# Kernel tuning notes

Measured on AMD Instinct MI355X. Metric: run time of the kernel, lower is better.

## Reference

```python
import jax, jax.numpy as jnp
import numpy as np

B_, L_, D_MODEL = 2, 4096, 1024
D_STATE, D_CONV, D_INNER = 64, 4, 2048
EPS = 1.1920929e-07  # torch.finfo(float32).eps, nn.RMSNorm default


def setup_inputs() -> dict:
    key = jax.random.key(0)
    ks = jax.random.split(key, 8)
    s = 0.02
    x = jax.random.normal(ks[0], (B_, L_, D_MODEL), jnp.float32)
    W_in = jax.random.normal(ks[1], (D_MODEL, 2 * D_INNER), jnp.float32) * s
    conv_w = jax.random.normal(ks[2], (D_INNER, 1, D_CONV), jnp.float32) * s  # depthwise (O,I/g,K)
    conv_b = jnp.zeros((D_INNER,), jnp.float32)
    W_x = jax.random.normal(ks[3], (D_INNER, 2 * D_STATE + D_INNER), jnp.float32) * s
    W_dt = jax.random.normal(ks[4], (D_INNER, D_INNER), jnp.float32) * s
    b_dt = jnp.zeros((D_INNER,), jnp.float32)
    A_log = jnp.log(jnp.tile(jnp.arange(1, D_STATE + 1, dtype=jnp.float32)[None, :], (D_INNER, 1)))
    D_param = jnp.ones((D_INNER,), jnp.float32)
    W_out = jax.random.normal(ks[5], (D_INNER, D_MODEL), jnp.float32) * s
    norm_w = jnp.ones((D_INNER,), jnp.float32)
    return dict(x=x, W_in=W_in, conv_w=conv_w, conv_b=conv_b, W_x=W_x, W_dt=W_dt,
                b_dt=b_dt, A_log=A_log, D_param=D_param, W_out=W_out, norm_w=norm_w)


def selective_scan(x_conv, dt, A, B_ssm, C_ssm, D_param):
    # x_conv,dt: (B,L,d_inner); A:(d_inner,d_state); B_ssm,C_ssm:(B,L,d_state)
    dt = jax.nn.softplus(dt)

    def step(h, inp):
        dt_t, B_t, C_t, x_t = inp  # (B,di),(B,ds),(B,ds),(B,di)
        dA = jnp.exp(dt_t[:, :, None] * A[None, :, :])           # (B,di,ds)
        h = dA * h + (dt_t * x_t)[:, :, None] * B_t[:, None, :]  # (B,di,ds)
        y = jnp.einsum('bds,bs->bd', h, C_t)                     # (B,di)
        return h, y

    h0 = jnp.zeros((x_conv.shape[0], A.shape[0], A.shape[1]), x_conv.dtype)
    xs = (jnp.moveaxis(dt, 1, 0), jnp.moveaxis(B_ssm, 1, 0),
          jnp.moveaxis(C_ssm, 1, 0), jnp.moveaxis(x_conv, 1, 0))
    _, ys = jax.lax.scan(step, h0, xs)
    y = jnp.moveaxis(ys, 0, 1)  # (B,L,d_inner)
    return y + x_conv * D_param[None, None, :]


def reference(x, W_in, conv_w, conv_b, W_x, W_dt, b_dt, A_log, D_param, W_out, norm_w):
    xz = x @ W_in                                    # (B,L,2*d_inner)
    x_ssm, z = jnp.split(xz, 2, axis=-1)
    # causal depthwise conv1d: left-pad d_conv-1 == torch pad-both-then-slice[:L]
    xc = jnp.swapaxes(x_ssm, 1, 2)                   # (B,d_inner,L)
    xc = jax.lax.conv_general_dilated(
        xc, conv_w, window_strides=(1,), padding=[(D_CONV - 1, 0)],
        dimension_numbers=('NCH', 'OIH', 'NCH'), feature_group_count=D_INNER)
    xc = xc + conv_b[None, :, None]
    xc = jax.nn.silu(jnp.swapaxes(xc, 1, 2))         # (B,L,d_inner)
    dbc = xc @ W_x                                   # (B,L,2*d_state+d_inner)
    B_ssm = dbc[..., :D_STATE]
    C_ssm = dbc[..., D_STATE:2 * D_STATE]
    dt = dbc[..., 2 * D_STATE:] @ W_dt + b_dt
    A = -jnp.exp(A_log)
    y = selective_scan(xc, dt, A, B_ssm, C_ssm, D_param)
    # RMSNorm then gate
    y = y * jax.lax.rsqrt(jnp.mean(y * y, axis=-1, keepdims=True) + EPS) * norm_w
    y = y * jax.nn.silu(z)
    return y @ W_out
```

## Files before the change

### kernel.cpp

```cpp
#include <hip/hip_runtime.h>
#include <hip/hip_bf16.h>

#define L_SEQ   4096
#define DMODEL  1024
#define DINNER  2048
#define DSTATE  64
#define NB      2
#define DPB     128
#define DBCS    2304
#define NROWS   (NB * L_SEQ)

typedef unsigned short u16;
typedef __attribute__((ext_vector_type(8))) short bf16x8;
typedef __attribute__((ext_vector_type(4))) float f32x4;
typedef __attribute__((ext_vector_type(2))) float f32x2;

__device__ __forceinline__ float silu_f(float x)  { return x / (1.f + __expf(-x)); }
__device__ __forceinline__ float softplus_f(float x) {
    return x > 15.f ? x : __logf(1.f + __expf(x));
}
__device__ __forceinline__ float bf2f(u16 u) { return __uint_as_float(((unsigned)u) << 16); }
__device__ __forceinline__ u16 f2bf(float f) {
    __hip_bfloat16 h = __float2bfloat16(f);
    return *reinterpret_cast<u16*>(&h);
}
__device__ __forceinline__ unsigned pack2(float a, float b) {
    return (unsigned)f2bf(a) | ((unsigned)f2bf(b) << 16);
}

__global__ __launch_bounds__(256) void f32_to_bf16_kernel(
    const float* __restrict__ in, u16* __restrict__ out)
{
    const int i = (blockIdx.x * 256 + threadIdx.x) * 4;
    float4 v = *reinterpret_cast<const float4*>(in + i);
    ushort4 o;
    o.x = f2bf(v.x); o.y = f2bf(v.y); o.z = f2bf(v.z); o.w = f2bf(v.w);
    *reinterpret_cast<ushort4*>(out + i) = o;
}

__global__ __launch_bounds__(256) void transpose_bf16_kernel(
    const float* __restrict__ W, u16* __restrict__ Wt, int K, int N)
{
    __shared__ float t[32][33];
    const int n0 = blockIdx.x * 32, k0 = blockIdx.y * 32;
    const int tx = threadIdx.x & 31, ty = threadIdx.x >> 5;
    #pragma unroll
    for (int i = 0; i < 32; i += 8)
        t[ty + i][tx] = W[(size_t)(k0 + ty + i) * N + n0 + tx];
    __syncthreads();
    #pragma unroll
    for (int i = 0; i < 32; i += 8)
        Wt[(size_t)(n0 + ty + i) * K + k0 + tx] = f2bf(t[tx][ty + i]);
}

__global__ __launch_bounds__(256) void bias_cat_kernel(
    const float* __restrict__ b_dt, float* __restrict__ bias)
{
    const int i = blockIdx.x * 256 + threadIdx.x;
    float v = 0.f;
    if (i >= 128 && i < 128 + DINNER) v = b_dt[i - 128];
    bias[i] = v;
}

#define BAR()  asm volatile("s_barrier" ::: "memory")
#define WV(n)  asm volatile("s_waitcnt vmcnt(" #n ")" ::: "memory")
#define STG16(s, d) __builtin_amdgcn_global_load_lds( \
    (const __attribute__((address_space(1))) void*)(s), \
    (__attribute__((address_space(3))) void*)(d), 16, 0, 0)

template <typename TC, int ACT>
__global__ __launch_bounds__(512, 2) void gemm256(
    const u16* __restrict__ A, int lda,
    const u16* __restrict__ Bt, int ldb,
    TC* __restrict__ C, int ldc,
    int K, const float* __restrict__ bias)
{
    extern __shared__ char lds[];
    const int tid = threadIdx.x;
    const int l = tid & 63, w = tid >> 6;
    const int wm = w >> 2, wn = w & 3;
    const int lr = l & 15, lk = l >> 4;

    const int gx = gridDim.x;
    const int nwg = gx * gridDim.y;
    int wg = blockIdx.y * gx + blockIdx.x;
    wg = (wg & 7) * (nwg >> 3) + (wg >> 3);
    const int bm = (wg / gx) * 256, bn = (wg % gx) * 256;

    const size_t ldaB = (size_t)lda * 2, ldbB = (size_t)ldb * 2;
    const int gsw = (((l & 7) ^ (l >> 3)) << 4);
    const char* aSrc = (const char*)A + (size_t)(bm + w * 8 + (l >> 3)) * ldaB + gsw;
    const char* bSrc = (const char*)Bt + (size_t)(bn + w * 8 + (l >> 3)) * ldbB + gsw;
    const int csw0 = (lk * 16) ^ ((lr & 7) << 4);
    const int wdst = w * 1024;

    const int nk = K >> 6;
    f32x4 acc[8][4] = {};

    {
        STG16(aSrc + (size_t)(0 * 64) * ldaB, lds + 0 * 8192 + wdst);
        STG16(aSrc + (size_t)(2 * 64) * ldaB, lds + 2 * 8192 + wdst);
        STG16(bSrc + (size_t)(0 * 64) * ldbB, lds + 32768 + 0 * 8192 + wdst);
        STG16(bSrc + (size_t)(1 * 64) * ldbB, lds + 32768 + 1 * 8192 + wdst);
        STG16(bSrc + (size_t)(2 * 64) * ldbB, lds + 32768 + 2 * 8192 + wdst);
        STG16(bSrc + (size_t)(3 * 64) * ldbB, lds + 32768 + 3 * 8192 + wdst);
        STG16(aSrc + (size_t)(1 * 64) * ldaB, lds + 1 * 8192 + wdst);
        STG16(aSrc + (size_t)(3 * 64) * ldaB, lds + 3 * 8192 + wdst);
        WV(2);
        BAR();
    }

    for (int t = 0; t < nk; ++t) {
        const int p = t & 1;
        const char* Ar = lds + (p << 16);
        const char* Br = Ar + 32768;
        const int tn = (t + 1 < nk) ? t + 1 : t;
        char* dq = lds + (((t + 1) & 1) << 16);
        const size_t Tb = (size_t)tn << 7;
        const char* aS = aSrc + Tb;
        const char* bS = bSrc + Tb;

        bf16x8 a[4][2], bf[2][2];

        #pragma unroll
        for (int mi = 0; mi < 4; ++mi) {
            const int ro = (wm * 128 + mi * 16 + lr) * 128;
            a[mi][0] = *reinterpret_cast<const bf16x8*>(Ar + ro + csw0);
            a[mi][1] = *reinterpret_cast<const bf16x8*>(Ar + ro + (csw0 ^ 64));
        }
        #pragma unroll
        for (int ni = 0; ni < 2; ++ni) {
            const int ro = (wn * 64 + ni * 16 + lr) * 128;
            bf[ni][0] = *reinterpret_cast<const bf16x8*>(Br + ro + csw0);
            bf[ni][1] = *reinterpret_cast<const bf16x8*>(Br + ro + (csw0 ^ 64));
        }
        STG16(aS + (size_t)(0 * 64) * ldaB, dq + 0 * 8192 + wdst);
        STG16(aS + (size_t)(2 * 64) * ldaB, dq + 2 * 8192 + wdst);
        BAR();
        __builtin_amdgcn_s_setprio(1);
        #pragma unroll
        for (int mi = 0; mi < 4; ++mi)
            #pragma unroll
            for (int ni = 0; ni < 2; ++ni) {
                acc[mi][ni] = __builtin_amdgcn_mfma_f32_16x16x32_bf16(a[mi][0], bf[ni][0], acc[mi][ni], 0, 0, 0);
                acc[mi][ni] = __builtin_amdgcn_mfma_f32_16x16x32_bf16(a[mi][1], bf[ni][1], acc[mi][ni], 0, 0, 0);
            }
        __builtin_amdgcn_s_setprio(0);
        BAR();

        #pragma unroll
        for (int ni = 0; ni < 2; ++ni) {
            const int ro = (wn * 64 + (2 + ni) * 16 + lr) * 128;
            bf[ni][0] = *reinterpret_cast<const bf16x8*>(Br + ro + csw0);
            bf[ni][1] = *reinterpret_cast<const bf16x8*>(Br + ro + (csw0 ^ 64));
        }
        STG16(bS + (size_t)(0 * 64) * ldbB, dq + 32768 + 0 * 8192 + wdst);
        STG16(bS + (size_t)(1 * 64) * ldbB, dq + 32768 + 1 * 8192 + wdst);
        BAR();
        __builtin_amdgcn_s_setprio(1);
        #pragma unroll
        for (int mi = 0; mi < 4; ++mi)
            #pragma unroll
            for (int ni = 0; ni < 2; ++ni) {
                acc[mi][2 + ni] = __builtin_amdgcn_mfma_f32_16x16x32_bf16(a[mi][0], bf[ni][0], acc[mi][2 + ni], 0, 0, 0);
                acc[mi][2 + ni] = __builtin_amdgcn_mfma_f32_16x16x32_bf16(a[mi][1], bf[ni][1], acc[mi][2 + ni], 0, 0, 0);
            }
        __builtin_amdgcn_s_setprio(0);
        WV(4);
        BAR();

        #pragma unroll
        for (int mi = 0; mi < 4; ++mi) {
            const int ro = (wm * 128 + (4 + mi) * 16 + lr) * 128;
            a[mi][0] = *reinterpret_cast<const bf16x8*>(Ar + ro + csw0);
            a[mi][1] = *reinterpret_cast<const bf16x8*>(Ar + ro + (csw0 ^ 64));
        }
        STG16(bS + (size_t)(2 * 64) * ldbB, dq + 32768 + 2 * 8192 + wdst);
        STG16(bS + (size_t)(3 * 64) * ldbB, dq + 32768 + 3 * 8192 + wdst);
        BAR();
        __builtin_amdgcn_s_setprio(1);
        #pragma unroll
        for (int mi = 0; mi < 4; ++mi)
            #pragma unroll
            for (int ni = 0; ni < 2; ++ni) {
                acc[4 + mi][2 + ni] = __builtin_amdgcn_mfma_f32_16x16x32_bf16(a[mi][0], bf[ni][0], acc[4 + mi][2 + ni], 0, 0, 0);
                acc[4 + mi][2 + ni] = __builtin_amdgcn_mfma_f32_16x16x32_bf16(a[mi][1], bf[ni][1], acc[4 + mi][2 + ni], 0, 0, 0);
            }
        __builtin_amdgcn_s_setprio(0);
        BAR();

        #pragma unroll
        for (int ni = 0; ni < 2; ++ni) {
            const int ro = (wn * 64 + ni * 16 + lr) * 128;
            bf[ni][0] = *reinterpret_cast<const bf16x8*>(Br + ro + csw0);
            bf[ni][1] = *reinterpret_cast<const bf16x8*>(Br + ro + (csw0 ^ 64));
        }
        STG16(aS + (size_t)(1 * 64) * ldaB, dq + 1 * 8192 + wdst);
        STG16(aS + (size_t)(3 * 64) * ldaB, dq + 3 * 8192 + wdst);
        BAR();
        __builtin_amdgcn_s_setprio(1);
        #pragma unroll
        for (int mi = 0; mi < 4; ++mi)
            #pragma unroll
            for (int ni = 0; ni < 2; ++ni) {
                acc[4 + mi][ni] = __builtin_amdgcn_mfma_f32_16x16x32_bf16(a[mi][0], bf[ni][0], acc[4 + mi][ni], 0, 0, 0);
                acc[4 + mi][ni] = __builtin_amdgcn_mfma_f32_16x16x32_bf16(a[mi][1], bf[ni][1], acc[4 + mi][ni], 0, 0, 0);
            }
        __builtin_amdgcn_s_setprio(0);
        WV(2);
        BAR();
    }

    float bv[4];
    if (bias) {
        #pragma unroll
        for (int ni = 0; ni < 4; ++ni) bv[ni] = bias[bn + wn * 64 + ni * 16 + lr];
    }
    #pragma unroll
    for (int mi = 0; mi < 8; ++mi) {
        #pragma unroll
        for (int ni = 0; ni < 4; ++ni) {
            #pragma unroll
            for (int r = 0; r < 4; ++r) {
                const int row = bm + wm * 128 + mi * 16 + lk * 4 + r;
                const int col = bn + wn * 64 + ni * 16 + lr;
                float v = acc[mi][ni][r];
                if (bias) v += bv[ni];
                if constexpr (ACT == 2) { if (col >= 128) v = softplus_f(v); }
                if constexpr (sizeof(TC) == 4) C[(size_t)row * ldc + col] = v;
                else                           C[(size_t)row * ldc + col] = f2bf(v);
            }
        }
    }
}

__global__ __launch_bounds__(256) void conv_silu_kernel(
    const u16* __restrict__ xz, const float* __restrict__ cw,
    const float* __restrict__ cb, u16* __restrict__ xc)
{
    const int idx8 = blockIdx.x * 256 + threadIdx.x;
    const int db  = (idx8 & 255) << 3;
    const int row = idx8 >> 8;
    const int l   = row & (L_SEQ - 1);

    float v[4][8];
    #pragma unroll
    for (int k = 0; k < 4; ++k) {
        const int ll = l - 3 + k;
        if (ll >= 0) {
            uint4 u = *reinterpret_cast<const uint4*>(xz + (size_t)(row - 3 + k) * 4096 + db);
            v[k][0]=bf2f((u16)(u.x&0xffff)); v[k][1]=bf2f((u16)(u.x>>16));
            v[k][2]=bf2f((u16)(u.y&0xffff)); v[k][3]=bf2f((u16)(u.y>>16));
            v[k][4]=bf2f((u16)(u.z&0xffff)); v[k][5]=bf2f((u16)(u.z>>16));
            v[k][6]=bf2f((u16)(u.w&0xffff)); v[k][7]=bf2f((u16)(u.w>>16));
        } else {
            #pragma unroll
            for (int j = 0; j < 8; ++j) v[k][j] = 0.f;
        }
    }
    float acc[8];
    {
        float4 c0 = *reinterpret_cast<const float4*>(cb + db);
        float4 c1 = *reinterpret_cast<const float4*>(cb + db + 4);
        acc[0]=c0.x; acc[1]=c0.y; acc[2]=c0.z; acc[3]=c0.w;
        acc[4]=c1.x; acc[5]=c1.y; acc[6]=c1.z; acc[7]=c1.w;
    }
    #pragma unroll
    for (int j = 0; j < 8; ++j) {
        const float4 wv = reinterpret_cast<const float4*>(cw)[db + j];
        acc[j] = fmaf(v[0][j], wv.x, acc[j]);
        acc[j] = fmaf(v[1][j], wv.y, acc[j]);
        acc[j] = fmaf(v[2][j], wv.z, acc[j]);
        acc[j] = fmaf(v[3][j], wv.w, acc[j]);
    }
    uint4 o;
    o.x = pack2(silu_f(acc[0]), silu_f(acc[1]));
    o.y = pack2(silu_f(acc[2]), silu_f(acc[3]));
    o.z = pack2(silu_f(acc[4]), silu_f(acc[5]));
    o.w = pack2(silu_f(acc[6]), silu_f(acc[7]));
    *reinterpret_cast<uint4*>(xc + (size_t)row * 2048 + db) = o;
}


__device__ __forceinline__ int a_pattern_check_half(
    const float* A_log, int d, int base, float& A0)
{
    A0 = -__expf(A_log[d * DSTATE]);
    int ok = 1;
    #pragma unroll
    for (int j = 0; j < 32; ++j) {
        const int s = base + j;
        const float As = -__expf(A_log[d * DSTATE + s]);
        ok &= (fabsf(As - A0 * (float)(s + 1)) <= 1e-3f * (float)(s + 1));
    }
    return ok;
}

#define UNPACK8(dstp, u)  do {                                             \
    float4 _a, _b;                                                         \
    _a.x=bf2f((u16)((u).x&0xffff)); _a.y=bf2f((u16)((u).x>>16));           \
    _a.z=bf2f((u16)((u).y&0xffff)); _a.w=bf2f((u16)((u).y>>16));           \
    _b.x=bf2f((u16)((u).z&0xffff)); _b.y=bf2f((u16)((u).z>>16));           \
    _b.z=bf2f((u16)((u).w&0xffff)); _b.w=bf2f((u16)((u).w>>16));           \
    *reinterpret_cast<float4*>(dstp) = _a;                                 \
    *reinterpret_cast<float4*>((dstp) + 4) = _b;                           \
} while (0)

__global__ __launch_bounds__(256) void scan_phase1(
    const u16* __restrict__ xc,
    const u16* __restrict__ dbc,
    const float* __restrict__ A_log,
    float* __restrict__ hend, float* __restrict__ sumdt,
    int nchunk, int chunk)
{
    const int tid  = threadIdx.x;
    const int dl   = tid >> 1, half = tid & 1;
    const int base = half * 32;
    const int d0   = blockIdx.x * DPB;
    const int d    = d0 + dl;
    const int c = blockIdx.y, b = blockIdx.z;
    const int t0 = c * chunk;
    const size_t bL = (size_t)b * L_SEQ;

    __shared__ float dts_s[16][132];
    __shared__ float xcs_s[16][132];
    __shared__ float Bs_s[16][68];

    float A0;
    int fast = a_pattern_check_half(A_log, d, base, A0);
    fast = __syncthreads_and(fast);

    f32x2 h2[16];
    #pragma unroll
    for (int j = 0; j < 16; ++j) h2[j] = (f32x2){0.f, 0.f};
    float sd = 0.f;

    for (int ts = 0; ts < chunk; ts += 16) {
        __syncthreads();
        {
            const int rr = tid >> 4, cc = (tid & 15) * 8;
            const size_t row = bL + t0 + ts + rr;
            uint4 v = *reinterpret_cast<const uint4*>(dbc + row * DBCS + 128 + d0 + cc);
            UNPACK8(&dts_s[rr][cc], v);
            uint4 u = *reinterpret_cast<const uint4*>(xc + row * 2048 + d0 + cc);
            UNPACK8(&xcs_s[rr][cc], u);
        }
        if (tid < 128) {
            const int rb = tid >> 3, cb = (tid & 7) * 8;
            const size_t row = bL + t0 + ts + rb;
            uint4 v = *reinterpret_cast<const uint4*>(dbc + row * DBCS + cb);
            UNPACK8(&Bs_s[rb][cb], v);
        }
        __syncthreads();
        if (fast) {
            for (int r = 0; r < 16; ++r) {
                const float dts = dts_s[r][dl];
                const float xv  = xcs_s[r][dl];
                const float dtx = dts * xv;
                sd += dts;
                const float q  = __expf(A0 * dts);
                const float q2 = q * q, q3 = q2 * q, q4 = q2 * q2;
                const float q8 = q4 * q4, q16 = q8 * q8, q32 = q16 * q16;
                const float qb = half ? q32 : 1.f;
                f32x2 pA = {qb * q, qb * q2};
                f32x2 pB = {qb * q3, qb * q4};
                const f32x2 q44 = {q4, q4};
                const f32x2 dtx2 = {dtx, dtx};
                #pragma unroll
                for (int g = 0; g < 8; ++g) {
                    const f32x4 Bq = *reinterpret_cast<const f32x4*>(&Bs_s[r][base + g * 4]);
                    const f32x2 B01 = {Bq[0], Bq[1]};
                    const f32x2 B23 = {Bq[2], Bq[3]};
                    h2[2*g]   = pA * h2[2*g]   + B01 * dtx2;
                    h2[2*g+1] = pB * h2[2*g+1] + B23 * dtx2;
                    pA = pA * q44; pB = pB * q44;
                }
            }
        } else {
            float* hs = (float*)h2;
            for (int r = 0; r < 16; ++r) {
                const float dts = dts_s[r][dl];
                const float xv  = xcs_s[r][dl];
                const float dtx = dts * xv;
                sd += dts;
                #pragma unroll
                for (int j = 0; j < 32; ++j) {
                    const float a = __expf(-__expf(A_log[d * DSTATE + base + j]) * dts);
                    hs[j] = fmaf(a, hs[j], dtx * Bs_s[r][base + j]);
                }
            }
        }
    }
    const size_t cb64 = ((size_t)b * nchunk + c) * DSTATE;
    const float* hs = (const float*)h2;
    #pragma unroll
    for (int j = 0; j < 32; ++j) hend[(cb64 + base + j) * DINNER + d] = hs[j];
    if (half == 0) sumdt[((size_t)b * nchunk + c) * DINNER + d] = sd;
}

__global__ __launch_bounds__(256) void scan_phase2(
    float* __restrict__ hbuf, const float* __restrict__ sumdt,
    const float* __restrict__ A_log, int nchunk)
{
    const int idx = blockIdx.x * 256 + threadIdx.x;
    const int d = idx & (DINNER - 1);
    const int s = (idx >> 11) & (DSTATE - 1);
    const int b = idx >> 17;

    const float A = -__expf(A_log[d * DSTATE + s]);
    float h = 0.f;
    for (int c = 0; c < nchunk; ++c) {
        const size_t off = (((size_t)b * nchunk + c) * DSTATE + s) * DINNER + d;
        const float he = hbuf[off];
        const float ap = __expf(A * sumdt[((size_t)b * nchunk + c) * DINNER + d]);
        hbuf[off] = h;
        h = fmaf(ap, h, he);
    }
}

__global__ __launch_bounds__(256) void scan_phase3(
    u16* __restrict__ xc,
    const u16* __restrict__ dbc,
    const float* __restrict__ A_log,
    const float* __restrict__ hinit,
    const float* __restrict__ D_param,
    int nchunk, int chunk)
{
    const int tid  = threadIdx.x;
    const int dl   = tid >> 1, half = tid & 1;
    const int base = half * 32;
    const int d0   = blockIdx.x * DPB;
    const int d    = d0 + dl;
    const int c = blockIdx.y, b = blockIdx.z;
    const int t0 = c * chunk;
    const size_t bL = (size_t)b * L_SEQ;

    __shared__ float dts_s[16][132];
    __shared__ float xcs_s[16][132];
    __shared__ float BCs[16][132];

    float A0;
    int fast = a_pattern_check_half(A_log, d, base, A0);
    fast = __syncthreads_and(fast);

    f32x2 h2[16];
    {
        const size_t cb64 = ((size_t)b * nchunk + c) * DSTATE;
        float* hs = (float*)h2;
        #pragma unroll
        for (int j = 0; j < 32; ++j) hs[j] = hinit[(cb64 + base + j) * DINNER + d];
    }
    const float Dp = D_param[d];

    for (int ts = 0; ts < chunk; ts += 16) {
        __syncthreads();
        {
            const int rr = tid >> 4, cc = (tid & 15) * 8;
            const size_t row = bL + t0 + ts + rr;
            uint4 v = *reinterpret_cast<const uint4*>(dbc + row * DBCS + 128 + d0 + cc);
            UNPACK8(&dts_s[rr][cc], v);
            uint4 u = *reinterpret_cast<const uint4*>(xc + row * 2048 + d0 + cc);
            UNPACK8(&xcs_s[rr][cc], u);
            uint4 w = *reinterpret_cast<const uint4*>(dbc + row * DBCS + cc);
            UNPACK8(&BCs[rr][cc], w);
        }
        __syncthreads();
        if (fast) {
            for (int r = 0; r < 16; ++r) {
                const float dts = dts_s[r][dl];
                const float xv  = xcs_s[r][dl];
                const float dtx = dts * xv;
                const float q  = __expf(A0 * dts);
                const float q2 = q * q, q3 = q2 * q, q4 = q2 * q2;
                const float q8 = q4 * q4, q16 = q8 * q8, q32 = q16 * q16;
                const float qb = half ? q32 : 1.f;
                f32x2 pA = {qb * q, qb * q2};
                f32x2 pB = {qb * q3, qb * q4};
                const f32x2 q44 = {q4, q4};
                const f32x2 dtx2 = {dtx, dtx};
                f32x2 y2 = {0.f, 0.f};
                #pragma unroll
                for (int g = 0; g < 8; ++g) {
                    const f32x4 Bq = *reinterpret_cast<const f32x4*>(&BCs[r][base + g * 4]);
                    const f32x4 Cq = *reinterpret_cast<const f32x4*>(&BCs[r][64 + base + g * 4]);
                    const f32x2 B01 = {Bq[0], Bq[1]};
                    const f32x2 B23 = {Bq[2], Bq[3]};
                    const f32x2 C01 = {Cq[0], Cq[1]};
                    const f32x2 C23 = {Cq[2], Cq[3]};
                    h2[2*g]   = pA * h2[2*g]   + B01 * dtx2;
                    h2[2*g+1] = pB * h2[2*g+1] + B23 * dtx2;
                    y2 = h2[2*g] * C01 + y2;
                    y2 = h2[2*g+1] * C23 + y2;
                    pA = pA * q44; pB = pB * q44;
                }
                float y = y2.x + y2.y;
                const float yt = y + __shfl_xor(y, 1, 64);
                if (half == 0) {
                    const size_t row = bL + t0 + ts + r;
                    xc[row * 2048 + d] = f2bf(fmaf(xv, Dp, yt));
                }
            }
        } else {
            float* hs = (float*)h2;
            for (int r = 0; r < 16; ++r) {
                const float dts = dts_s[r][dl];
                const float xv  = xcs_s[r][dl];
                const float dtx = dts * xv;
                float y = 0.f;
                #pragma unroll
                for (int j = 0; j < 32; ++j) {
                    const float a = __expf(-__expf(A_log[d * DSTATE + base + j]) * dts);
                    hs[j] = fmaf(a, hs[j], dtx * BCs[r][base + j]);
                    y = fmaf(hs[j], BCs[r][64 + base + j], y);
                }
                const float yt = y + __shfl_xor(y, 1, 64);
                if (half == 0) {
                    const size_t row = bL + t0 + ts + r;
                    xc[row * 2048 + d] = f2bf(fmaf(xv, Dp, yt));
                }
            }
        }
    }
}

__global__ __launch_bounds__(256) void rms_gate_kernel(
    u16* __restrict__ y, const u16* __restrict__ xz,
    const float* __restrict__ norm_w)
{
    const int row = blockIdx.x;
    const int tid = threadIdx.x;
    const size_t ybase = (size_t)row * DINNER;
    const size_t zbase = (size_t)row * 4096 + DINNER;
    const int i8 = tid * 8;

    float yv[8];
    {
        uint4 u = *reinterpret_cast<const uint4*>(y + ybase + i8);
        yv[0]=bf2f((u16)(u.x&0xffff)); yv[1]=bf2f((u16)(u.x>>16));
        yv[2]=bf2f((u16)(u.y&0xffff)); yv[3]=bf2f((u16)(u.y>>16));
        yv[4]=bf2f((u16)(u.z&0xffff)); yv[5]=bf2f((u16)(u.z>>16));
        yv[6]=bf2f((u16)(u.w&0xffff)); yv[7]=bf2f((u16)(u.w>>16));
    }
    float ss = 0.f;
    #pragma unroll
    for (int j = 0; j < 8; ++j) ss = fmaf(yv[j], yv[j], ss);
    #pragma unroll
    for (int off = 32; off > 0; off >>= 1) ss += __shfl_down(ss, off, 64);
    __shared__ float sred[4];
    const int lane = tid & 63, wid = tid >> 6;
    if (lane == 0) sred[wid] = ss;
    __syncthreads();
    const float tot = sred[0] + sred[1] + sred[2] + sred[3];
    const float scale = rsqrtf(tot * (1.f / (float)DINNER) + 1.1920929e-07f);

    float zv[8];
    {
        uint4 u = *reinterpret_cast<const uint4*>(xz + zbase + i8);
        zv[0]=bf2f((u16)(u.x&0xffff)); zv[1]=bf2f((u16)(u.x>>16));
        zv[2]=bf2f((u16)(u.y&0xffff)); zv[3]=bf2f((u16)(u.y>>16));
        zv[4]=bf2f((u16)(u.z&0xffff)); zv[5]=bf2f((u16)(u.z>>16));
        zv[6]=bf2f((u16)(u.w&0xffff)); zv[7]=bf2f((u16)(u.w>>16));
    }
    float4 n0 = *reinterpret_cast<const float4*>(norm_w + i8);
    float4 n1 = *reinterpret_cast<const float4*>(norm_w + i8 + 4);
    const float nw[8] = {n0.x,n0.y,n0.z,n0.w,n1.x,n1.y,n1.z,n1.w};
    float o[8];
    #pragma unroll
    for (int j = 0; j < 8; ++j) o[j] = yv[j] * scale * nw[j] * silu_f(zv[j]);
    uint4 ov;
    ov.x = pack2(o[0], o[1]); ov.y = pack2(o[2], o[3]);
    ov.z = pack2(o[4], o[5]); ov.w = pack2(o[6], o[7]);
    *reinterpret_cast<uint4*>(y + ybase + i8) = ov;
}

extern "C" void kernel_launch(void* const* d_in, const int* in_sizes, int n_in,
                              void* d_out, int out_size, void* d_ws, size_t ws_size,
                              hipStream_t stream)
{
    const float* x       = (const float*)d_in[0];
    const float* W_in    = (const float*)d_in[1];
    const float* conv_w  = (const float*)d_in[2];
    const float* conv_b  = (const float*)d_in[3];
    const float* W_x     = (const float*)d_in[4];
    const float* W_dt    = (const float*)d_in[5];
    const float* b_dt    = (const float*)d_in[6];
    const float* A_log   = (const float*)d_in[7];
    const float* D_param = (const float*)d_in[8];
    const float* W_out   = (const float*)d_in[9];
    const float* norm_w  = (const float*)d_in[10];
    float* out = (float*)d_out;

    hipFuncSetAttribute(reinterpret_cast<const void*>(&gemm256<u16, 0>),
                        hipFuncAttributeMaxDynamicSharedMemorySize, 131072);
    hipFuncSetAttribute(reinterpret_cast<const void*>(&gemm256<u16, 2>),
                        hipFuncAttributeMaxDynamicSharedMemorySize, 131072);
    hipFuncSetAttribute(reinterpret_cast<const void*>(&gemm256<float, 0>),
                        hipFuncAttributeMaxDynamicSharedMemorySize, 131072);

    char* ws = (char*)d_ws;
    u16* xz  = (u16*)(ws);
    u16* xc  = (u16*)(ws + 67108864ull);
    u16* dbc = (u16*)(ws + 100663296ull);
    u16* xbf  = dbc;
    u16* Wxbf = xz;
    u16* Wt_out = (u16*)(ws + 138412032ull);
    float* bias2304 = (float*)(ws + 142606336ull);
    const size_t fixed_bytes = 142615552ull;
    const size_t per_chunk = 2ull * DSTATE * DINNER * 4 + 2ull * DINNER * 4;
    int nchunk = 32;
    while (nchunk > 1 && fixed_bytes + (size_t)nchunk * per_chunk > ws_size) nchunk >>= 1;
    const int chunk = L_SEQ / nchunk;
    float* hbuf = (float*)(ws + fixed_bytes);
    float* sdt  = (float*)(ws + fixed_bytes + (size_t)nchunk * 2ull * DSTATE * DINNER * 4);

    u16* Wt_in = (u16*)d_out;
    u16* Wt_x  = Wt_in + 4194304ull;
    u16* Wt_dt = Wt_x + 4718592ull;

    const int M = NROWS;

    f32_to_bf16_kernel<<<(M * DMODEL) / 1024, 256, 0, stream>>>(x, xbf);
    f32_to_bf16_kernel<<<(DINNER * 2176) / 1024, 256, 0, stream>>>(W_x, Wxbf);
    transpose_bf16_kernel<<<dim3(4096 / 32, 1024 / 32), 256, 0, stream>>>(W_in, Wt_in, 1024, 4096);
    transpose_bf16_kernel<<<dim3(4, 2048 / 32), 256, 0, stream>>>(W_x, Wt_x, 2048, 2176);
    transpose_bf16_kernel<<<dim3(2048 / 32, 2048 / 32), 256, 0, stream>>>(W_dt, Wt_dt, 2048, 2048);
    transpose_bf16_kernel<<<dim3(1024 / 32, 2048 / 32), 256, 0, stream>>>(W_out, Wt_out, 2048, 1024);
    bias_cat_kernel<<<9, 256, 0, stream>>>(b_dt, bias2304);
    hipMemsetAsync(Wt_x + 2176ull * 2048, 0, 128ull * 2048 * 2, stream);
    gemm256<u16, 0><<<dim3(2048 / 256, 2048 / 256), 512, 131072, stream>>>(
        Wt_dt, 2048, Wxbf + 128, 2176, Wt_x + 128ull * 2048, 2048, 2048, nullptr);

    gemm256<u16, 0><<<dim3(4096 / 256, M / 256), 512, 131072, stream>>>(
        xbf, DMODEL, Wt_in, DMODEL, xz, 4096, DMODEL, nullptr);
    conv_silu_kernel<<<(M * DINNER) / (256 * 8), 256, 0, stream>>>(xz, conv_w, conv_b, xc);
    gemm256<u16, 2><<<dim3(DBCS / 256, M / 256), 512, 131072, stream>>>(
        xc, DINNER, Wt_x, DINNER, dbc, DBCS, DINNER, bias2304);
    scan_phase1<<<dim3(DINNER / DPB, nchunk, NB), 256, 0, stream>>>(
        xc, dbc, A_log, hbuf, sdt, nchunk, chunk);
    scan_phase2<<<(NB * DINNER * DSTATE) / 256, 256, 0, stream>>>(hbuf, sdt, A_log, nchunk);
    scan_phase3<<<dim3(DINNER / DPB, nchunk, NB), 256, 0, stream>>>(
        xc, dbc, A_log, hbuf, D_param, nchunk, chunk);
    rms_gate_kernel<<<M, 256, 0, stream>>>(xc, xz, norm_w);
    gemm256<float, 0><<<dim3(1024 / 256, M / 256), 512, 131072, stream>>>(
        xc, DINNER, Wt_out, DINNER, out, DMODEL, DINNER, nullptr);
}
```

Measured before the change: 644.8 us.

## Split scan phase3 state across four threads and precompute A pattern flags

Scan phase3 now uses 512-thread blocks, with each channel's 64 states split across four lanes (16 each) instead of two. That halves per-thread register state and serial work per step, and the partial outputs are reduced with two xor shuffles. The staging loads are split so half the threads load dt/x and the other half load B/C. A new small kernel precomputes A0 and the geometric-pattern flag per channel once, so phase1 and phase3 no longer recompute 32 exps per thread. The cost is an extra launch, a second exp per step for the offset power, and more shuffle traffic.

```diff
diff --git a/kernel.cpp b/kernel.cpp
--- a/kernel.cpp
+++ b/kernel.cpp
@@ -60,6 +60,21 @@
     float v = 0.f;
     if (i >= 128 && i < 128 + DINNER) v = b_dt[i - 128];
     bias[i] = v;
+}
+
+__global__ __launch_bounds__(256) void a0_kernel(
+    const float* __restrict__ A_log, float* __restrict__ A0f,
+    unsigned char* __restrict__ okf)
+{
+    const int d = blockIdx.x * 256 + threadIdx.x;
+    const float A0 = -__expf(A_log[d * DSTATE]);
+    int ok = 1;
+    for (int s = 1; s < DSTATE; ++s) {
+        const float As = -__expf(A_log[d * DSTATE + s]);
+        ok &= (fabsf(As - A0 * (float)(s + 1)) <= 1e-3f * (float)(s + 1));
+    }
+    A0f[d] = A0;
+    okf[d] = (unsigned char)ok;
 }
 
 #define BAR()  asm volatile("s_barrier" ::: "memory")
@@ -282,20 +297,6 @@
 }
 
 
-__device__ __forceinline__ int a_pattern_check_half(
-    const float* A_log, int d, int base, float& A0)
-{
-    A0 = -__expf(A_log[d * DSTATE]);
-    int ok = 1;
-    #pragma unroll
-    for (int j = 0; j < 32; ++j) {
-        const int s = base + j;
-        const float As = -__expf(A_log[d * DSTATE + s]);
-        ok &= (fabsf(As - A0 * (float)(s + 1)) <= 1e-3f * (float)(s + 1));
-    }
-    return ok;
-}
-
 #define UNPACK8(dstp, u)  do {                                             \
     float4 _a, _b;                                                         \
     _a.x=bf2f((u16)((u).x&0xffff)); _a.y=bf2f((u16)((u).x>>16));           \
@@ -310,6 +311,7 @@
     const u16* __restrict__ xc,
     const u16* __restrict__ dbc,
     const float* __restrict__ A_log,
+    const float* __restrict__ A0f, const unsigned char* __restrict__ okf,
     float* __restrict__ hend, float* __restrict__ sumdt,
     int nchunk, int chunk)
 {
@@ -326,9 +328,8 @@
     __shared__ float xcs_s[16][132];
     __shared__ float Bs_s[16][68];
 
-    float A0;
-    int fast = a_pattern_check_half(A_log, d, base, A0);
-    fast = __syncthreads_and(fast);
+    const float A0 = A0f[d];
+    int fast = __syncthreads_and((int)okf[d]);
 
     f32x2 h2[16];
     #pragma unroll
@@ -418,17 +419,19 @@
     }
 }
 
-__global__ __launch_bounds__(256) void scan_phase3(
+__global__ __launch_bounds__(512, 8) void scan_phase3(
     u16* __restrict__ xc,
     const u16* __restrict__ dbc,
     const float* __restrict__ A_log,
+    const float* __restrict__ A0f, const unsigned char* __restrict__ okf,
     const float* __restrict__ hinit,
     const float* __restrict__ D_param,
     int nchunk, int chunk)
 {
     const int tid  = threadIdx.x;
-    const int dl   = tid >> 1, half = tid & 1;
-    const int base = half * 32;
+    const int dl   = tid >> 2, qtr = tid & 3;
+    const int base = qtr * 16;
+    const float kof = (float)(base + 1);
     const int d0   = blockIdx.x * DPB;
     const int d    = d0 + dl;
     const int c = blockIdx.y, b = blockIdx.z;
@@ -439,30 +442,34 @@
     __shared__ float xcs_s[16][132];
     __shared__ float BCs[16][132];
 
-    float A0;
-    int fast = a_pattern_check_half(A_log, d, base, A0);
-    fast = __syncthreads_and(fast);
-
-    f32x2 h2[16];
+    const float A0 = A0f[d];
+    int fast = __syncthreads_and((int)okf[d]);
+
+    f32x2 h2[8];
     {
         const size_t cb64 = ((size_t)b * nchunk + c) * DSTATE;
         float* hs = (float*)h2;
         #pragma unroll
-        for (int j = 0; j < 32; ++j) hs[j] = hinit[(cb64 + base + j) * DINNER + d];
+        for (int j = 0; j < 16; ++j) hs[j] = hinit[(cb64 + base + j) * DINNER + d];
     }
     const float Dp = D_param[d];
+
+    const int st = tid & 255;
+    const int rr = st >> 4, cc = (st & 15) * 8;
 
     for (int ts = 0; ts < chunk; ts += 16) {
         __syncthreads();
         {
-            const int rr = tid >> 4, cc = (tid & 15) * 8;
-            const size_t row = bL + t0 + ts + rr;
-            uint4 v = *reinterpret_cast<const uint4*>(dbc + row * DBCS + 128 + d0 + cc);
-            UNPACK8(&dts_s[rr][cc], v);
-            uint4 u = *reinterpret_cast<const uint4*>(xc + row * 2048 + d0 + cc);
-            UNPACK8(&xcs_s[rr][cc], u);
-            uint4 w = *reinterpret_cast<const uint4*>(dbc + row * DBCS + cc);
-            UNPACK8(&BCs[rr][cc], w);
+            const size_t srow = bL + t0 + ts + rr;
+            if (tid < 256) {
+                uint4 v = *reinterpret_cast<const uint4*>(dbc + srow * DBCS + 128 + d0 + cc);
+                UNPACK8(&dts_s[rr][cc], v);
+                uint4 u = *reinterpret_cast<const uint4*>(xc + srow * 2048 + d0 + cc);
+                UNPACK8(&xcs_s[rr][cc], u);
+            } else {
+                uint4 w = *reinterpret_cast<const uint4*>(dbc + srow * DBCS + cc);
+                UNPACK8(&BCs[rr][cc], w);
+            }
         }
         __syncthreads();
         if (fast) {
@@ -470,17 +477,17 @@
                 const float dts = dts_s[r][dl];
                 const float xv  = xcs_s[r][dl];
                 const float dtx = dts * xv;
-                const float q  = __expf(A0 * dts);
-                const float q2 = q * q, q3 = q2 * q, q4 = q2 * q2;
-                const float q8 = q4 * q4, q16 = q8 * q8, q32 = q16 * q16;
-                const float qb = half ? q32 : 1.f;
-                f32x2 pA = {qb * q, qb * q2};
-                f32x2 pB = {qb * q3, qb * q4};
+                const float ad = A0 * dts;
+                const float q  = __expf(ad);
+                const float e2 = __expf(ad * kof);
+                const float q2 = q * q, q4 = q2 * q2;
+                f32x2 pA = {e2, e2 * q};
+                f32x2 pB = {e2 * q2, e2 * q2 * q};
                 const f32x2 q44 = {q4, q4};
                 const f32x2 dtx2 = {dtx, dtx};
                 f32x2 y2 = {0.f, 0.f};
                 #pragma unroll
-                for (int g = 0; g < 8; ++g) {
+                for (int g = 0; g < 4; ++g) {
                     const f32x4 Bq = *reinterpret_cast<const f32x4*>(&BCs[r][base + g * 4]);
                     const f32x4 Cq = *reinterpret_cast<const f32x4*>(&BCs[r][64 + base + g * 4]);
                     const f32x2 B01 = {Bq[0], Bq[1]};
@@ -494,10 +501,11 @@
                     pA = pA * q44; pB = pB * q44;
                 }
                 float y = y2.x + y2.y;
-                const float yt = y + __shfl_xor(y, 1, 64);
-                if (half == 0) {
+                y += __shfl_xor(y, 1, 64);
+                y += __shfl_xor(y, 2, 64);
+                if (qtr == 0) {
                     const size_t row = bL + t0 + ts + r;
-                    xc[row * 2048 + d] = f2bf(fmaf(xv, Dp, yt));
+                    xc[row * 2048 + d] = f2bf(fmaf(xv, Dp, y));
                 }
             }
         } else {
@@ -508,15 +516,16 @@
                 const float dtx = dts * xv;
                 float y = 0.f;
                 #pragma unroll
-                for (int j = 0; j < 32; ++j) {
+                for (int j = 0; j < 16; ++j) {
                     const float a = __expf(-__expf(A_log[d * DSTATE + base + j]) * dts);
                     hs[j] = fmaf(a, hs[j], dtx * BCs[r][base + j]);
                     y = fmaf(hs[j], BCs[r][64 + base + j], y);
                 }
-                const float yt = y + __shfl_xor(y, 1, 64);
-                if (half == 0) {
+                y += __shfl_xor(y, 1, 64);
+                y += __shfl_xor(y, 2, 64);
+                if (qtr == 0) {
                     const size_t row = bL + t0 + ts + r;
-                    xc[row * 2048 + d] = f2bf(fmaf(xv, Dp, yt));
+                    xc[row * 2048 + d] = f2bf(fmaf(xv, Dp, y));
                 }
             }
         }
@@ -605,7 +614,9 @@
     u16* Wxbf = xz;
     u16* Wt_out = (u16*)(ws + 138412032ull);
     float* bias2304 = (float*)(ws + 142606336ull);
-    const size_t fixed_bytes = 142615552ull;
+    float* A0f = (float*)(ws + 142615552ull);
+    unsigned char* okf = (unsigned char*)(ws + 142623744ull);
+    const size_t fixed_bytes = 142625792ull;
     const size_t per_chunk = 2ull * DSTATE * DINNER * 4 + 2ull * DINNER * 4;
     int nchunk = 32;
     while (nchunk > 1 && fixed_bytes + (size_t)nchunk * per_chunk > ws_size) nchunk >>= 1;
@@ -626,6 +637,7 @@
     transpose_bf16_kernel<<<dim3(2048 / 32, 2048 / 32), 256, 0, stream>>>(W_dt, Wt_dt, 2048, 2048);
     transpose_bf16_kernel<<<dim3(1024 / 32, 2048 / 32), 256, 0, stream>>>(W_out, Wt_out, 2048, 1024);
     bias_cat_kernel<<<9, 256, 0, stream>>>(b_dt, bias2304);
+    a0_kernel<<<DINNER / 256, 256, 0, stream>>>(A_log, A0f, okf);
     hipMemsetAsync(Wt_x + 2176ull * 2048, 0, 128ull * 2048 * 2, stream);
     gemm256<u16, 0><<<dim3(2048 / 256, 2048 / 256), 512, 131072, stream>>>(
         Wt_dt, 2048, Wxbf + 128, 2176, Wt_x + 128ull * 2048, 2048, 2048, nullptr);
@@ -636,10 +648,10 @@
     gemm256<u16, 2><<<dim3(DBCS / 256, M / 256), 512, 131072, stream>>>(
         xc, DINNER, Wt_x, DINNER, dbc, DBCS, DINNER, bias2304);
     scan_phase1<<<dim3(DINNER / DPB, nchunk, NB), 256, 0, stream>>>(
-        xc, dbc, A_log, hbuf, sdt, nchunk, chunk);
+        xc, dbc, A_log, A0f, okf, hbuf, sdt, nchunk, chunk);
     scan_phase2<<<(NB * DINNER * DSTATE) / 256, 256, 0, stream>>>(hbuf, sdt, A_log, nchunk);
-    scan_phase3<<<dim3(DINNER / DPB, nchunk, NB), 256, 0, stream>>>(
-        xc, dbc, A_log, hbuf, D_param, nchunk, chunk);
+    scan_phase3<<<dim3(DINNER / DPB, nchunk, NB), 512, 0, stream>>>(
+        xc, dbc, A_log, A0f, okf, hbuf, D_param, nchunk, chunk);
     rms_gate_kernel<<<M, 256, 0, stream>>>(xc, xz, norm_w);
     gemm256<float, 0><<<dim3(1024 / 256, M / 256), 512, 131072, stream>>>(
         xc, DINNER, Wt_out, DINNER, out, DMODEL, DINNER, nullptr);
```

After: 719.8 us. 1.12x slower.
